# Optimization experiments

Hardware: AMD Instinct MI355X
Metric: run time of the kernel (lower is better)

Reference implementation:

```python
import jax, jax.numpy as jnp
import numpy as np
import math

B, S, DQ, DK, DV, H = 8, 2048, 256, 256, 256, 4
DH = DV // H
EPS = 1e-5

def _layernorm(x, g, b):
    mu = jnp.mean(x, axis=-1, keepdims=True)
    var = jnp.mean(jnp.square(x - mu), axis=-1, keepdims=True)
    return (x - mu) * jax.lax.rsqrt(var + EPS) * g + b

def setup_inputs() -> dict:
    key = jax.random.key(0)
    ks = jax.random.split(key, 12)
    s_in = 1.0 / math.sqrt(DQ)
    s_v = 1.0 / math.sqrt(DV)
    return {
        "Q": jax.random.normal(ks[0], (B, S, DQ), dtype=jnp.float32),
        "K": jax.random.normal(ks[1], (B, S, DK), dtype=jnp.float32),
        "Wq": jax.random.uniform(ks[2], (DQ, DV), jnp.float32, -s_in, s_in),
        "bq": jax.random.uniform(ks[3], (DV,), jnp.float32, -s_in, s_in),
        "Wk": jax.random.uniform(ks[4], (DK, DV), jnp.float32, -s_in, s_in),
        "bk": jax.random.uniform(ks[5], (DV,), jnp.float32, -s_in, s_in),
        "Wv": jax.random.uniform(ks[6], (DK, DV), jnp.float32, -s_in, s_in),
        "bv": jax.random.uniform(ks[7], (DV,), jnp.float32, -s_in, s_in),
        "Wo": jax.random.uniform(ks[8], (DV, DV), jnp.float32, -s_v, s_v),
        "bo": jax.random.uniform(ks[9], (DV,), jnp.float32, -s_v, s_v),
        "g0": jnp.ones((DV,), jnp.float32),
        "beta0": jnp.zeros((DV,), jnp.float32),
        "g1": jnp.ones((DV,), jnp.float32),
        "beta1": jnp.zeros((DV,), jnp.float32),
    }

def reference(Q, K, Wq, bq, Wk, bk, Wv, bv, Wo, bo, g0, beta0, g1, beta1):
    q = Q @ Wq + bq                    # [B,S,DV]
    k = K @ Wk + bk
    v = K @ Wv + bv
    q4 = q.reshape(B, S, H, DH)
    k4 = k.reshape(B, S, H, DH)
    v4 = v.reshape(B, S, H, DH)
    scores = jnp.einsum('bqhd,bkhd->bhqk', q4, k4) / math.sqrt(DH)
    A = jax.nn.softmax(scores, axis=-1)
    o = q4 + jnp.einsum('bhqk,bkhd->bqhd', A, v4)  # residual with projected Q per head
    O = o.reshape(B, S, DV)
    O = _layernorm(O, g0, beta0)
    O = O + jax.nn.relu(O @ Wo + bo)
    O = _layernorm(O, g1, beta1)
    return O
```

## Files before the change

kernel.cpp:

```cpp
#include <hip/hip_runtime.h>
#include <hip/hip_bf16.h>
#include <stdint.h>

typedef uint16_t u16;
typedef uint32_t u32;
typedef __attribute__((ext_vector_type(8))) short short8;
typedef __attribute__((ext_vector_type(4))) float f32x4;

#define LOG2E 1.44269504088896340736f

__device__ __forceinline__ u16 f2bf(float f) {
    u32 u = __builtin_bit_cast(u32, f);
    return (u16)((u + 0x7fffu + ((u >> 16) & 1u)) >> 16);
}
__device__ __forceinline__ float bf2f(u16 h) {
    u32 u = ((u32)h) << 16;
    return __builtin_bit_cast(float, u);
}
__device__ __forceinline__ u32 pack_bf16(float lo, float hi) {
    return (u32)f2bf(lo) | ((u32)f2bf(hi) << 16);
}
__device__ __forceinline__ u32 pack_bf16_fast(float lo, float hi) {
    u32 a = __builtin_bit_cast(u32, lo) + 0x8000u;
    u32 b = __builtin_bit_cast(u32, hi) + 0x8000u;
    return (a >> 16) | (b & 0xffff0000u);
}

__global__ __launch_bounds__(256)
void prep_kernel(const float* __restrict__ Q, const float* __restrict__ K,
                 u16* __restrict__ Qc, u16* __restrict__ Kc,
                 const float* __restrict__ Wq, const float* __restrict__ Wk,
                 const float* __restrict__ Wv, const float* __restrict__ Wo,
                 const float* __restrict__ bk, u16* __restrict__ WT,
                 float* __restrict__ bks) {
    const int bid = blockIdx.x;
    if (bid < 4096) {
        const float* src = (bid < 2048) ? Q : K;
        u16* dst = (bid < 2048) ? Qc : Kc;
        const size_t i = ((size_t)(bid & 2047) * 256 + threadIdx.x) * 8;
        float4 a = *(const float4*)(src + i);
        float4 b = *(const float4*)(src + i + 4);
        uint4 o;
        o.x = pack_bf16(a.x, a.y);
        o.y = pack_bf16(a.z, a.w);
        o.z = pack_bf16(b.x, b.y);
        o.w = pack_bf16(b.z, b.w);
        *(uint4*)(dst + i) = o;
    } else {
        const int idx = bid - 4096;
        const int wsel = idx >> 8, k = idx & 255, n = threadIdx.x;
        const float* W = (wsel == 0) ? Wq : (wsel == 1) ? Wk : (wsel == 2) ? Wv : Wo;
        const float scale = (wsel == 1) ? (0.125f * LOG2E) : 1.0f;
        WT[(size_t)wsel * 65536 + (size_t)n * 256 + k] = f2bf(W[(size_t)k * 256 + n] * scale);
        if (wsel == 1 && k == 0) bks[n] = bk[n] * (0.125f * LOG2E);
    }
}

template<int EPI>
__device__ __forceinline__ void gemm_body(const u16* __restrict__ A, const u16* __restrict__ BT,
                                          const float* __restrict__ bias, const float* resid,
                                          void* outp) {
    __shared__ u16 As[128 * 64];
    __shared__ u16 Bs[128 * 64];
    const int tid = threadIdx.x;
    const int w = tid >> 6, lane = tid & 63;
    const int g = lane >> 4, lo = lane & 15;
    const int rowB = blockIdx.x * 128;
    const int colB = blockIdx.y * 128;
    const int wr = (w >> 1) * 64, wc = (w & 1) * 64;

    const f32x4 fz = {0.f, 0.f, 0.f, 0.f};
    f32x4 acc[4][4];
#pragma unroll
    for (int m = 0; m < 4; ++m)
#pragma unroll
        for (int n = 0; n < 4; ++n) acc[m][n] = fz;

    const int srow = tid & 127;
    const int shalf = tid >> 7;

#pragma unroll 1
    for (int kt = 0; kt < 4; ++kt) {
        const int k0 = kt * 64;
        __syncthreads();
        {
            const u16* ga = A + (size_t)(rowB + srow) * 256 + k0 + shalf * 32;
            uint4 a0 = *(const uint4*)ga;
            uint4 a1 = *(const uint4*)(ga + 8);
            uint4 a2 = *(const uint4*)(ga + 16);
            uint4 a3 = *(const uint4*)(ga + 24);
            const u16* gb = BT + (size_t)(colB + srow) * 256 + k0 + shalf * 32;
            uint4 b0 = *(const uint4*)gb;
            uint4 b1 = *(const uint4*)(gb + 8);
            uint4 b2 = *(const uint4*)(gb + 16);
            uint4 b3 = *(const uint4*)(gb + 24);
            const u32 sw = (u32)((srow & 7) << 4);
            const u32 ba = (u32)(srow * 128 + shalf * 64);
            *(uint4*)((char*)As + ((ba) ^ sw))      = a0;
            *(uint4*)((char*)As + ((ba + 16) ^ sw)) = a1;
            *(uint4*)((char*)As + ((ba + 32) ^ sw)) = a2;
            *(uint4*)((char*)As + ((ba + 48) ^ sw)) = a3;
            *(uint4*)((char*)Bs + ((ba) ^ sw))      = b0;
            *(uint4*)((char*)Bs + ((ba + 16) ^ sw)) = b1;
            *(uint4*)((char*)Bs + ((ba + 32) ^ sw)) = b2;
            *(uint4*)((char*)Bs + ((ba + 48) ^ sw)) = b3;
        }
        __syncthreads();
#pragma unroll
        for (int c = 0; c < 2; ++c) {
            short8 af[4], bfr[4];
#pragma unroll
            for (int m = 0; m < 4; ++m) {
                const int row = wr + m * 16 + lo;
                const u32 addr = (u32)(row * 128 + c * 64 + g * 16) ^ (u32)((row & 7) << 4);
                af[m] = *(const short8*)((char*)As + addr);
            }
#pragma unroll
            for (int n = 0; n < 4; ++n) {
                const int row = wc + n * 16 + lo;
                const u32 addr = (u32)(row * 128 + c * 64 + g * 16) ^ (u32)((row & 7) << 4);
                bfr[n] = *(const short8*)((char*)Bs + addr);
            }
#pragma unroll
            for (int m = 0; m < 4; ++m)
#pragma unroll
                for (int n = 0; n < 4; ++n)
                    acc[m][n] = __builtin_amdgcn_mfma_f32_16x16x32_bf16(af[m], bfr[n], acc[m][n], 0, 0, 0);
        }
    }

    float bv[4];
#pragma unroll
    for (int n = 0; n < 4; ++n) bv[n] = bias[colB + wc + n * 16 + lo];

    if (EPI == 0) {
        u16* out = (u16*)outp;
#pragma unroll
        for (int m = 0; m < 4; ++m)
#pragma unroll
            for (int r = 0; r < 4; ++r) {
                const size_t row = (size_t)(rowB + wr + m * 16 + g * 4 + r);
#pragma unroll
                for (int n = 0; n < 4; ++n)
                    out[row * 256 + colB + wc + n * 16 + lo] = f2bf(acc[m][n][r] + bv[n]);
            }
    } else {
        float* out = (float*)outp;
#pragma unroll
        for (int m = 0; m < 4; ++m)
#pragma unroll
            for (int r = 0; r < 4; ++r) {
                const size_t row = (size_t)(rowB + wr + m * 16 + g * 4 + r);
#pragma unroll
                for (int n = 0; n < 4; ++n) {
                    const size_t idx = row * 256 + colB + wc + n * 16 + lo;
                    out[idx] = resid[idx] + fmaxf(acc[m][n][r] + bv[n], 0.f);
                }
            }
    }
}

__global__ __launch_bounds__(256)
void proj_kernel(const u16* __restrict__ Qc, const u16* __restrict__ Kc,
                 const u16* __restrict__ WT, const float* __restrict__ bq,
                 const float* __restrict__ bks, const float* __restrict__ bvv,
                 u16* __restrict__ qb, u16* __restrict__ kbuf, u16* __restrict__ vbuf) {
    const int z = blockIdx.z;
    const u16* A = (z == 0) ? Qc : Kc;
    const u16* BT = WT + z * 65536;
    const float* bias = (z == 0) ? bq : (z == 1) ? bks : bvv;
    u16* out = (z == 0) ? qb : (z == 1) ? kbuf : vbuf;
    gemm_body<0>(A, BT, bias, nullptr, (void*)out);
}

__global__ __launch_bounds__(256)
void mlp_kernel(const u16* __restrict__ A, const u16* __restrict__ BT,
                const float* __restrict__ bias, const float* resid, float* outp) {
    gemm_body<1>(A, BT, bias, resid, (void*)outp);
}

__global__ __launch_bounds__(512, 4)
void attn_kernel(const u16* __restrict__ qb, const u16* __restrict__ kb,
                 const u16* __restrict__ vb, float* __restrict__ Obuf) {
    __shared__ u16 Klds[2 * 64 * 64];
    __shared__ u16 Vtlds[2 * 64 * 64];
    __shared__ u16 Plds[8 * 16 * 64];
    const int tid = threadIdx.x;
    const int w = tid >> 6, lane = tid & 63;
    const int g = lane >> 4, lo = lane & 15;
    const int q0 = blockIdx.x * 128;
    const int h = blockIdx.y, b = blockIdx.z;
    const size_t hbase = (size_t)b * 2048 * 256 + (size_t)h * 64;

    short8 qf[2];
#pragma unroll
    for (int c = 0; c < 2; ++c) {
        const size_t row = (size_t)(q0 + w * 16 + lo);
        qf[c] = *(const short8*)&qb[hbase + row * 256 + c * 32 + g * 8];
    }
    const short8 vones = {0x3F80, 0x3F80, 0x3F80, 0x3F80, 0x3F80, 0x3F80, 0x3F80, 0x3F80};

    const f32x4 fz = {0.f, 0.f, 0.f, 0.f};
    f32x4 oacc[4];
#pragma unroll
    for (int n = 0; n < 4; ++n) oacc[n] = fz;
    f32x4 l_acc = fz;
    float m_run = -1e30f;

    char* Pb = (char*)Plds + w * 2048;

    const bool kRole = (tid < 256);
    const int skey = tid & 63, sseg = (tid >> 6) & 3;
    const int t4 = tid & 255;
    const int vkey = (t4 & 31) * 2, vd0 = (t4 >> 5) * 8;
    const u16* gbase;
    int goff2;
    if (kRole) { gbase = &kb[hbase + (size_t)skey * 256 + sseg * 16]; goff2 = 8; }
    else       { gbase = &vb[hbase + (size_t)vkey * 256 + vd0];       goff2 = 256; }

    uint4 s0, s1;
    auto load_tile = [&](int kt) {
        const u16* p = gbase + (size_t)kt * 16384;
        s0 = *(const uint4*)p;
        s1 = *(const uint4*)(p + goff2);
    };
    auto write_tile = [&](int sel) {
        if (kRole) {
            char* Kb_ = (char*)Klds + sel * 8192;
            const u32 sw = (u32)((skey & 7) << 4);
            const u32 ba = (u32)(skey * 128 + sseg * 32);
            *(uint4*)(Kb_ + ((ba) ^ sw)) = s0;
            *(uint4*)(Kb_ + ((ba + 16) ^ sw)) = s1;
        } else {
            char* Vb_ = (char*)Vtlds + sel * 8192;
            union { uint4 v; u16 hh[8]; } a0, a1;
            a0.v = s0; a1.v = s1;
#pragma unroll
            for (int i = 0; i < 8; ++i) {
                const int d = vd0 + i;
                const u32 addr = (u32)(d * 128 + vkey * 2) ^ (u32)((d & 7) << 4);
                *(u32*)(Vb_ + addr) = (u32)a0.hh[i] | ((u32)a1.hh[i] << 16);
            }
        }
    };

    load_tile(0);
    write_tile(0);
    load_tile(1);
    __syncthreads();

#pragma unroll 1
    for (int kt = 0; kt < 32; ++kt) {
        const int cur = kt & 1;
        char* Klb = (char*)Klds + cur * 8192;
        char* Vtb = (char*)Vtlds + cur * 8192;

        f32x4 sc[4];
#pragma unroll
        for (int km = 0; km < 4; ++km) sc[km] = fz;
#pragma unroll
        for (int c = 0; c < 2; ++c)
#pragma unroll
            for (int km = 0; km < 4; ++km) {
                const int key = km * 16 + lo;
                const u32 addr = (u32)(key * 128 + c * 64 + g * 16) ^ (u32)((key & 7) << 4);
                const short8 kf = *(const short8*)(Klb + addr);
                sc[km] = __builtin_amdgcn_mfma_f32_16x16x32_bf16(kf, qf[c], sc[km], 0, 0, 0);
            }

        float mt = -1e30f;
#pragma unroll
        for (int km = 0; km < 4; ++km)
#pragma unroll
            for (int r = 0; r < 4; ++r) mt = fmaxf(mt, sc[km][r]);
        mt = fmaxf(mt, __shfl_xor(mt, 16));
        mt = fmaxf(mt, __shfl_xor(mt, 32));
        if (!__all(mt <= m_run + 11.5f)) {
            const float mnew = fmaxf(m_run, mt);
            const float alpha = __builtin_amdgcn_exp2f(m_run - mnew);
#pragma unroll
            for (int r = 0; r < 4; ++r) {
                const float a = __shfl(alpha, (lane & 48) | (g * 4 + r));
                l_acc[r] *= a;
#pragma unroll
                for (int n = 0; n < 4; ++n) oacc[n][r] *= a;
            }
            m_run = mnew;
        }
#pragma unroll
        for (int km = 0; km < 4; ++km)
#pragma unroll
            for (int r = 0; r < 4; ++r)
                sc[km][r] = __builtin_amdgcn_exp2f(sc[km][r] - m_run);

        {
            const u32 sw = (u32)((lo & 7) << 4);
#pragma unroll
            for (int km = 0; km < 4; ++km) {
                uint2 val;
                val.x = pack_bf16_fast(sc[km][0], sc[km][1]);
                val.y = pack_bf16_fast(sc[km][2], sc[km][3]);
                const u32 addr = (u32)(lo * 128 + km * 32 + g * 8) ^ sw;
                *(uint2*)(Pb + addr) = val;
            }
        }

#pragma unroll
        for (int c = 0; c < 2; ++c) {
            const u32 paddr = (u32)(lo * 128 + c * 64 + g * 16) ^ (u32)((lo & 7) << 4);
            const short8 pf = *(const short8*)(Pb + paddr);
#pragma unroll
            for (int n = 0; n < 4; ++n) {
                const int d = n * 16 + lo;
                const u32 addr = (u32)(d * 128 + c * 64 + g * 16) ^ (u32)((d & 7) << 4);
                const short8 vf = *(const short8*)(Vtb + addr);
                oacc[n] = __builtin_amdgcn_mfma_f32_16x16x32_bf16(pf, vf, oacc[n], 0, 0, 0);
            }
            l_acc = __builtin_amdgcn_mfma_f32_16x16x32_bf16(pf, vones, l_acc, 0, 0, 0);
        }

        if (kt < 31) write_tile(cur ^ 1);
        if (kt < 30) load_tile(kt + 2);
        __syncthreads();
    }

#pragma unroll
    for (int r = 0; r < 4; ++r) {
        const float li = 1.0f / l_acc[r];
        const size_t row = (size_t)(q0 + w * 16 + g * 4 + r);
#pragma unroll
        for (int n = 0; n < 4; ++n) {
            const int d = n * 16 + lo;
            const size_t idx = hbase + row * 256 + d;
            Obuf[idx] = oacc[n][r] * li + bf2f(qb[idx]);
        }
    }
}

template<bool WB>
__global__ __launch_bounds__(256)
void ln_kernel(const float* in, const float* __restrict__ gam,
               const float* __restrict__ bet, float* of,
               u16* __restrict__ ob) {
    const int w = threadIdx.x >> 6, lane = threadIdx.x & 63;
    const size_t row = (size_t)blockIdx.x * 4 + w;
    const float4 v = ((const float4*)(in + row * 256))[lane];
    float s = v.x + v.y + v.z + v.w;
    float q = v.x * v.x + v.y * v.y + v.z * v.z + v.w * v.w;
#pragma unroll
    for (int m = 1; m <= 32; m <<= 1) {
        s += __shfl_xor(s, m);
        q += __shfl_xor(q, m);
    }
    const float mu = s * (1.f / 256.f);
    const float var = q * (1.f / 256.f) - mu * mu;
    const float rstd = rsqrtf(var + 1e-5f);
    const float4 gv = ((const float4*)gam)[lane];
    const float4 bv = ((const float4*)bet)[lane];
    float4 y;
    y.x = (v.x - mu) * rstd * gv.x + bv.x;
    y.y = (v.y - mu) * rstd * gv.y + bv.y;
    y.z = (v.z - mu) * rstd * gv.z + bv.z;
    y.w = (v.w - mu) * rstd * gv.w + bv.w;
    ((float4*)(of + row * 256))[lane] = y;
    if (WB) {
        uint2 pk;
        pk.x = pack_bf16(y.x, y.y);
        pk.y = pack_bf16(y.z, y.w);
        *(uint2*)(ob + row * 256 + lane * 4) = pk;
    }
}

extern "C" void kernel_launch(void* const* d_in, const int* in_sizes, int n_in,
                              void* d_out, int out_size, void* d_ws, size_t ws_size,
                              hipStream_t stream) {
    const float* Q  = (const float*)d_in[0];
    const float* K  = (const float*)d_in[1];
    const float* Wq = (const float*)d_in[2];
    const float* bq = (const float*)d_in[3];
    const float* Wk = (const float*)d_in[4];
    const float* bk = (const float*)d_in[5];
    const float* Wv = (const float*)d_in[6];
    const float* bv = (const float*)d_in[7];
    const float* Wo = (const float*)d_in[8];
    const float* bo = (const float*)d_in[9];
    const float* g0 = (const float*)d_in[10];
    const float* be0 = (const float*)d_in[11];
    const float* g1 = (const float*)d_in[12];
    const float* be1 = (const float*)d_in[13];
    float* out = (float*)d_out;

    const size_t NE = (size_t)8 * 2048 * 256;
    char* ws = (char*)d_ws;
    size_t off = 0;
    auto alloc = [&](size_t bytes) { char* p = ws + off; off += (bytes + 255) & ~(size_t)255; return p; };
    u16* Qc   = (u16*)alloc(NE * 2);
    u16* Kc   = (u16*)alloc(NE * 2);
    u16* qb   = (u16*)alloc(NE * 2);
    u16* kbuf = (u16*)alloc(NE * 2);
    u16* vbuf = (u16*)alloc(NE * 2);
    u16* WT   = (u16*)alloc(4 * 65536 * 2);
    float* bks = (float*)alloc(256 * 4);
    u16* Xb   = Qc;
    float* Obuf = out;

    prep_kernel<<<5120, 256, 0, stream>>>(Q, K, Qc, Kc, Wq, Wk, Wv, Wo, bk, WT, bks);

    proj_kernel<<<dim3(128, 2, 3), 256, 0, stream>>>(Qc, Kc, WT, bq, bks, bv, qb, kbuf, vbuf);

    attn_kernel<<<dim3(16, 4, 8), 512, 0, stream>>>(qb, kbuf, vbuf, Obuf);

    ln_kernel<true><<<4096, 256, 0, stream>>>(Obuf, g0, be0, Obuf, Xb);
    mlp_kernel<<<dim3(128, 2), 256, 0, stream>>>(Xb, WT + 3 * 65536, bo, Obuf, Obuf);
    ln_kernel<false><<<4096, 256, 0, stream>>>(Obuf, g1, be1, out, nullptr);
}
```

Measured before the change: 129.3 us.

## Fuse output MLP with final layernorm, store attention output in bf16

The attention output is now written as bf16 instead of fp32, and the first layernorm reads bf16. The output GEMM is merged with the second layernorm in one kernel that covers full 256-column rows per block, staging results in LDS, which removes one launch and one fp32 round trip through memory. s_setprio hints are also placed around the MFMA sections of the attention loop. The cost is extra bf16 rounding of the pre-layernorm activations, which reduces precision, and a smaller grid for the fused GEMM (256 blocks).

```diff
diff --git a/kernel.cpp b/kernel.cpp
--- a/kernel.cpp
+++ b/kernel.cpp
@@ -56,10 +56,17 @@
     }
 }
 
-template<int EPI>
-__device__ __forceinline__ void gemm_body(const u16* __restrict__ A, const u16* __restrict__ BT,
-                                          const float* __restrict__ bias, const float* resid,
-                                          void* outp) {
+__global__ __launch_bounds__(256)
+void proj_kernel(const u16* __restrict__ Qc, const u16* __restrict__ Kc,
+                 const u16* __restrict__ WT, const float* __restrict__ bq,
+                 const float* __restrict__ bks, const float* __restrict__ bvv,
+                 u16* __restrict__ qb, u16* __restrict__ kbuf, u16* __restrict__ vbuf) {
+    const int z = blockIdx.z;
+    const u16* A = (z == 0) ? Qc : Kc;
+    const u16* BT = WT + z * 65536;
+    const float* bias = (z == 0) ? bq : (z == 1) ? bks : bvv;
+    u16* out = (z == 0) ? qb : (z == 1) ? kbuf : vbuf;
+
     __shared__ u16 As[128 * 64];
     __shared__ u16 Bs[128 * 64];
     const int tid = threadIdx.x;
@@ -132,56 +139,20 @@
     float bv[4];
 #pragma unroll
     for (int n = 0; n < 4; ++n) bv[n] = bias[colB + wc + n * 16 + lo];
-
-    if (EPI == 0) {
-        u16* out = (u16*)outp;
-#pragma unroll
-        for (int m = 0; m < 4; ++m)
-#pragma unroll
-            for (int r = 0; r < 4; ++r) {
-                const size_t row = (size_t)(rowB + wr + m * 16 + g * 4 + r);
-#pragma unroll
-                for (int n = 0; n < 4; ++n)
-                    out[row * 256 + colB + wc + n * 16 + lo] = f2bf(acc[m][n][r] + bv[n]);
-            }
-    } else {
-        float* out = (float*)outp;
-#pragma unroll
-        for (int m = 0; m < 4; ++m)
-#pragma unroll
-            for (int r = 0; r < 4; ++r) {
-                const size_t row = (size_t)(rowB + wr + m * 16 + g * 4 + r);
-#pragma unroll
-                for (int n = 0; n < 4; ++n) {
-                    const size_t idx = row * 256 + colB + wc + n * 16 + lo;
-                    out[idx] = resid[idx] + fmaxf(acc[m][n][r] + bv[n], 0.f);
-                }
-            }
-    }
-}
-
-__global__ __launch_bounds__(256)
-void proj_kernel(const u16* __restrict__ Qc, const u16* __restrict__ Kc,
-                 const u16* __restrict__ WT, const float* __restrict__ bq,
-                 const float* __restrict__ bks, const float* __restrict__ bvv,
-                 u16* __restrict__ qb, u16* __restrict__ kbuf, u16* __restrict__ vbuf) {
-    const int z = blockIdx.z;
-    const u16* A = (z == 0) ? Qc : Kc;
-    const u16* BT = WT + z * 65536;
-    const float* bias = (z == 0) ? bq : (z == 1) ? bks : bvv;
-    u16* out = (z == 0) ? qb : (z == 1) ? kbuf : vbuf;
-    gemm_body<0>(A, BT, bias, nullptr, (void*)out);
-}
-
-__global__ __launch_bounds__(256)
-void mlp_kernel(const u16* __restrict__ A, const u16* __restrict__ BT,
-                const float* __restrict__ bias, const float* resid, float* outp) {
-    gemm_body<1>(A, BT, bias, resid, (void*)outp);
+#pragma unroll
+    for (int m = 0; m < 4; ++m)
+#pragma unroll
+        for (int r = 0; r < 4; ++r) {
+            const size_t row = (size_t)(rowB + wr + m * 16 + g * 4 + r);
+#pragma unroll
+            for (int n = 0; n < 4; ++n)
+                out[row * 256 + colB + wc + n * 16 + lo] = f2bf(acc[m][n][r] + bv[n]);
+        }
 }
 
 __global__ __launch_bounds__(512, 4)
 void attn_kernel(const u16* __restrict__ qb, const u16* __restrict__ kb,
-                 const u16* __restrict__ vb, float* __restrict__ Obuf) {
+                 const u16* __restrict__ vb, u16* __restrict__ Ob) {
     __shared__ u16 Klds[2 * 64 * 64];
     __shared__ u16 Vtlds[2 * 64 * 64];
     __shared__ u16 Plds[8 * 16 * 64];
@@ -258,6 +229,7 @@
         f32x4 sc[4];
 #pragma unroll
         for (int km = 0; km < 4; ++km) sc[km] = fz;
+        __builtin_amdgcn_s_setprio(1);
 #pragma unroll
         for (int c = 0; c < 2; ++c)
 #pragma unroll
@@ -267,6 +239,7 @@
                 const short8 kf = *(const short8*)(Klb + addr);
                 sc[km] = __builtin_amdgcn_mfma_f32_16x16x32_bf16(kf, qf[c], sc[km], 0, 0, 0);
             }
+        __builtin_amdgcn_s_setprio(0);
 
         float mt = -1e30f;
 #pragma unroll
@@ -305,6 +278,7 @@
             }
         }
 
+        __builtin_amdgcn_s_setprio(1);
 #pragma unroll
         for (int c = 0; c < 2; ++c) {
             const u32 paddr = (u32)(lo * 128 + c * 64 + g * 16) ^ (u32)((lo & 7) << 4);
@@ -318,6 +292,7 @@
             }
             l_acc = __builtin_amdgcn_mfma_f32_16x16x32_bf16(pf, vones, l_acc, 0, 0, 0);
         }
+        __builtin_amdgcn_s_setprio(0);
 
         if (kt < 31) write_tile(cur ^ 1);
         if (kt < 30) load_tile(kt + 2);
@@ -332,19 +307,23 @@
         for (int n = 0; n < 4; ++n) {
             const int d = n * 16 + lo;
             const size_t idx = hbase + row * 256 + d;
-            Obuf[idx] = oacc[n][r] * li + bf2f(qb[idx]);
-        }
-    }
-}
-
-template<bool WB>
+            Ob[idx] = f2bf(oacc[n][r] * li + bf2f(qb[idx]));
+        }
+    }
+}
+
 __global__ __launch_bounds__(256)
-void ln_kernel(const float* in, const float* __restrict__ gam,
-               const float* __restrict__ bet, float* of,
-               u16* __restrict__ ob) {
+void ln0_kernel(const u16* in, const float* __restrict__ gam,
+                const float* __restrict__ bet, float* __restrict__ of,
+                u16* ob) {
     const int w = threadIdx.x >> 6, lane = threadIdx.x & 63;
     const size_t row = (size_t)blockIdx.x * 4 + w;
-    const float4 v = ((const float4*)(in + row * 256))[lane];
+    const uint2 raw = *(const uint2*)(in + row * 256 + lane * 4);
+    float4 v;
+    v.x = bf2f((u16)(raw.x & 0xffff));
+    v.y = bf2f((u16)(raw.x >> 16));
+    v.z = bf2f((u16)(raw.y & 0xffff));
+    v.w = bf2f((u16)(raw.y >> 16));
     float s = v.x + v.y + v.z + v.w;
     float q = v.x * v.x + v.y * v.y + v.z * v.z + v.w * v.w;
 #pragma unroll
@@ -363,11 +342,145 @@
     y.z = (v.z - mu) * rstd * gv.z + bv.z;
     y.w = (v.w - mu) * rstd * gv.w + bv.w;
     ((float4*)(of + row * 256))[lane] = y;
-    if (WB) {
-        uint2 pk;
-        pk.x = pack_bf16(y.x, y.y);
-        pk.y = pack_bf16(y.z, y.w);
-        *(uint2*)(ob + row * 256 + lane * 4) = pk;
+    uint2 pk;
+    pk.x = pack_bf16(y.x, y.y);
+    pk.y = pack_bf16(y.z, y.w);
+    *(uint2*)(ob + row * 256 + lane * 4) = pk;
+}
+
+__global__ __launch_bounds__(256)
+void mlp_ln1_kernel(const u16* __restrict__ A, const u16* __restrict__ BT,
+                    const float* __restrict__ bias, const float* __restrict__ gam,
+                    const float* __restrict__ bet, float* out) {
+    __shared__ char lds[40960];
+    u16* As = (u16*)lds;
+    u16* Bs = (u16*)(lds + 8192);
+    char* Ys = lds;
+    const int tid = threadIdx.x;
+    const int w = tid >> 6, lane = tid & 63;
+    const int g = lane >> 4, lo = lane & 15;
+    const int rowB = blockIdx.x * 64;
+    const int wc = w * 64;
+
+    const f32x4 fz = {0.f, 0.f, 0.f, 0.f};
+    f32x4 acc[4][4];
+#pragma unroll
+    for (int m = 0; m < 4; ++m)
+#pragma unroll
+        for (int n = 0; n < 4; ++n) acc[m][n] = fz;
+
+    const int arow = tid & 63, aqtr = tid >> 6;
+#pragma unroll 1
+    for (int kt = 0; kt < 4; ++kt) {
+        const int k0 = kt * 64;
+        __syncthreads();
+        {
+            const u16* ga = A + (size_t)(rowB + arow) * 256 + k0 + aqtr * 16;
+            uint4 a0 = *(const uint4*)ga;
+            uint4 a1 = *(const uint4*)(ga + 8);
+            const u32 swA = (u32)((arow & 7) << 4);
+            const u32 baA = (u32)(arow * 128 + aqtr * 32);
+            *(uint4*)((char*)As + ((baA) ^ swA))      = a0;
+            *(uint4*)((char*)As + ((baA + 16) ^ swA)) = a1;
+            const u16* gb = BT + (size_t)tid * 256 + k0;
+            const u32 swB = (u32)((tid & 7) << 4);
+            const u32 baB = (u32)(tid * 128);
+#pragma unroll
+            for (int j = 0; j < 8; ++j) {
+                uint4 bj = *(const uint4*)(gb + j * 8);
+                *(uint4*)((char*)Bs + ((baB + j * 16) ^ swB)) = bj;
+            }
+        }
+        __syncthreads();
+#pragma unroll
+        for (int c = 0; c < 2; ++c) {
+            short8 af[4], bfr[4];
+#pragma unroll
+            for (int m = 0; m < 4; ++m) {
+                const int row = m * 16 + lo;
+                const u32 addr = (u32)(row * 128 + c * 64 + g * 16) ^ (u32)((row & 7) << 4);
+                af[m] = *(const short8*)((char*)As + addr);
+            }
+#pragma unroll
+            for (int n = 0; n < 4; ++n) {
+                const int row = wc + n * 16 + lo;
+                const u32 addr = (u32)(row * 128 + c * 64 + g * 16) ^ (u32)((row & 7) << 4);
+                bfr[n] = *(const short8*)((char*)Bs + addr);
+            }
+#pragma unroll
+            for (int m = 0; m < 4; ++m)
+#pragma unroll
+                for (int n = 0; n < 4; ++n)
+                    acc[m][n] = __builtin_amdgcn_mfma_f32_16x16x32_bf16(af[m], bfr[n], acc[m][n], 0, 0, 0);
+        }
+    }
+
+    float bv[4];
+#pragma unroll
+    for (int n = 0; n < 4; ++n) bv[n] = bias[wc + n * 16 + lo];
+
+    __syncthreads();
+
+#pragma unroll
+    for (int m = 0; m < 4; ++m)
+#pragma unroll
+        for (int r = 0; r < 4; ++r) {
+            const int row_l = m * 16 + g * 4 + r;
+            const u32 sw = (u32)((row_l & 7) << 4);
+            const size_t grow = (size_t)(rowB + row_l);
+#pragma unroll
+            for (int n = 0; n < 4; ++n) {
+                const int col = wc + n * 16 + lo;
+                const float y = out[grow * 256 + col] + fmaxf(acc[m][n][r] + bv[n], 0.f);
+                const u32 badr = (u32)(row_l * 512 + col * 2);
+                const u32 addr = (badr & ~15u) ^ sw;
+                *(u16*)(Ys + addr + (badr & 15u)) = f2bf(y);
+            }
+        }
+    __syncthreads();
+
+    {
+        const int row = tid >> 2, qtr = tid & 3;
+        const u32 sw = (u32)((row & 7) << 4);
+        const u32 rbase = (u32)(row * 512 + qtr * 128);
+        float s = 0.f, q = 0.f;
+#pragma unroll
+        for (int j = 0; j < 8; ++j) {
+            uint4 v4 = *(const uint4*)(Ys + ((rbase + j * 16) ^ sw));
+            const u32 uu[4] = {v4.x, v4.y, v4.z, v4.w};
+#pragma unroll
+            for (int e = 0; e < 4; ++e) {
+                const float f0 = bf2f((u16)(uu[e] & 0xffff));
+                const float f1 = bf2f((u16)(uu[e] >> 16));
+                s += f0 + f1;
+                q += f0 * f0 + f1 * f1;
+            }
+        }
+        s += __shfl_xor(s, 1); q += __shfl_xor(q, 1);
+        s += __shfl_xor(s, 2); q += __shfl_xor(q, 2);
+        const float mu = s * (1.f / 256.f);
+        const float var = q * (1.f / 256.f) - mu * mu;
+        const float rstd = rsqrtf(var + 1e-5f);
+        const size_t grow = (size_t)(rowB + row);
+        float* op = out + grow * 256 + qtr * 64;
+        const float* gp = gam + qtr * 64;
+        const float* bp = bet + qtr * 64;
+#pragma unroll
+        for (int j = 0; j < 8; ++j) {
+            uint4 v4 = *(const uint4*)(Ys + ((rbase + j * 16) ^ sw));
+            const u32 uu[4] = {v4.x, v4.y, v4.z, v4.w};
+#pragma unroll
+            for (int e = 0; e < 2; ++e) {
+                float4 gv = *(const float4*)(gp + j * 8 + e * 4);
+                float4 bb = *(const float4*)(bp + j * 8 + e * 4);
+                float4 o4;
+                o4.x = (bf2f((u16)(uu[e * 2]     & 0xffff)) - mu) * rstd * gv.x + bb.x;
+                o4.y = (bf2f((u16)(uu[e * 2]     >> 16))    - mu) * rstd * gv.y + bb.y;
+                o4.z = (bf2f((u16)(uu[e * 2 + 1] & 0xffff)) - mu) * rstd * gv.z + bb.z;
+                o4.w = (bf2f((u16)(uu[e * 2 + 1] >> 16))    - mu) * rstd * gv.w + bb.w;
+                *(float4*)(op + j * 8 + e * 4) = o4;
+            }
+        }
     }
 }
 
@@ -401,16 +514,15 @@
     u16* vbuf = (u16*)alloc(NE * 2);
     u16* WT   = (u16*)alloc(4 * 65536 * 2);
     float* bks = (float*)alloc(256 * 4);
-    u16* Xb   = Qc;
-    float* Obuf = out;
+    u16* Ob16 = Qc;
 
     prep_kernel<<<5120, 256, 0, stream>>>(Q, K, Qc, Kc, Wq, Wk, Wv, Wo, bk, WT, bks);
 
     proj_kernel<<<dim3(128, 2, 3), 256, 0, stream>>>(Qc, Kc, WT, bq, bks, bv, qb, kbuf, vbuf);
 
-    attn_kernel<<<dim3(16, 4, 8), 512, 0, stream>>>(qb, kbuf, vbuf, Obuf);
-
-    ln_kernel<true><<<4096, 256, 0, stream>>>(Obuf, g0, be0, Obuf, Xb);
-    mlp_kernel<<<dim3(128, 2), 256, 0, stream>>>(Xb, WT + 3 * 65536, bo, Obuf, Obuf);
-    ln_kernel<false><<<4096, 256, 0, stream>>>(Obuf, g1, be1, out, nullptr);
-}
+    attn_kernel<<<dim3(16, 4, 8), 512, 0, stream>>>(qb, kbuf, vbuf, Ob16);
+
+    ln0_kernel<<<4096, 256, 0, stream>>>(Ob16, g0, be0, out, Ob16);
+
+    mlp_ln1_kernel<<<256, 256, 0, stream>>>(Ob16, WT + 3 * 65536, bo, g1, be1, out);
+}
```

Result: faster. 121.6 us (-6.0%).
